# Optimization experiments

Measured on AMD Instinct MI355X. Metric: run time of the kernel, lower is better.

Reference implementation:

```python
import jax, jax.numpy as jnp
import numpy as np

DN = ('NCDHW', 'OIDHW', 'NCDHW')

def conv3(x, w):
    # 3x3x3 VALID stencil conv: [1,1,D+2,H+2,W+2] -> [1,1,D,H,W]
    return jax.lax.conv_general_dilated(x, w, (1, 1, 1), 'VALID', dimension_numbers=DN)

def conv_res(x, w):
    # 2x2x2 stride-2 restriction
    return jax.lax.conv_general_dilated(x, w, (2, 2, 2), 'VALID', dimension_numbers=DN)

def prol(x):
    for ax in (2, 3, 4):
        x = jnp.repeat(x, 2, axis=ax)
    return x

def with_halo(x, factor=1.0):
    # apply_BC_* + halo_exchange on one device: edge-replicate a 1-cell halo,
    # optionally scaled by `factor` (apply_BC_u uses -1.0 -> no-slip wall).
    p = jnp.pad(x, ((0, 0), (0, 0), (1, 1), (1, 1), (1, 1)), mode='edge')
    if factor != 1.0:
        interior = jnp.pad(jnp.ones_like(x), ((0, 0), (0, 0), (1, 1), (1, 1), (1, 1)))
        p = p * (interior + factor * (1.0 - interior))
    return p

def pad0(x):
    # apply_BC_cw: zero halo for the multigrid correction
    return jnp.pad(x, ((0, 0), (0, 0), (1, 1), (1, 1), (1, 1)))


def setup_inputs() -> dict:
    key = jax.random.key(0)
    ks = jax.random.split(key, 12)
    D = 128
    shp = (1, 1, D, D, D)
    f32 = jnp.float32
    values_u = jax.random.normal(ks[0], shp, f32)
    values_v = jax.random.normal(ks[1], shp, f32)
    values_w = jax.random.normal(ks[2], shp, f32)
    values_p = jax.random.normal(ks[3], shp, f32)
    sigma = jax.random.uniform(ks[4], shp, f32)
    kshape = (1, 1, 3, 3, 3)
    w_xadv = 0.1 * jax.random.normal(ks[5], kshape, f32)
    w_yadv = 0.1 * jax.random.normal(ks[6], kshape, f32)
    w_zadv = 0.1 * jax.random.normal(ks[7], kshape, f32)
    w_diff = 0.1 * jax.random.normal(ks[8], kshape, f32)
    wA = 0.1 * jax.random.normal(ks[9], kshape, f32)
    wA = wA.at[0, 0, 1, 1, 1].add(-6.0)  # Laplacian-like diagonal so Jacobi division is stable
    w_res = 0.1 * jax.random.normal(ks[10], (1, 1, 2, 2, 2), f32)
    dt = 0.05 * jnp.ones((1,), f32)
    return dict(values_u=values_u, values_v=values_v, values_w=values_w,
                values_p=values_p, sigma=sigma, w_xadv=w_xadv, w_yadv=w_yadv,
                w_zadv=w_zadv, w_diff=w_diff, wA=wA, w_res=w_res, dt=dt,
                iteration=2, nlevel=9)


def reference(values_u, values_v, values_w, values_p, sigma, w_xadv, w_yadv,
              w_zadv, w_diff, wA, w_res, dt, iteration, nlevel):
    diag = wA[0, 0, 1, 1, 1]
    xadv = lambda t: conv3(t, w_xadv)
    yadv = lambda t: conv3(t, w_yadv)
    zadv = lambda t: conv3(t, w_zadv)
    diff = lambda t: conv3(t, w_diff)
    A = lambda t: conv3(t, wA)

    def solid(a, b, c):
        d = 1.0 + dt * sigma
        return a / d, b / d, c / d

    def PG(uu, vv, ww, u, v, w):
        # k_u/k_v/k_w are ones; k_uu/k_vv/k_ww are their BC+halo versions (also ones)
        k_h = with_halo(jnp.ones_like(u))
        k_u = 0.5 * (diff(uu) + diff(uu * k_h) - u * diff(k_h))
        k_v = 0.5 * (diff(vv) + diff(vv * k_h) - v * diff(k_h))
        k_w = 0.5 * (diff(ww) + diff(ww * k_h) - w * diff(k_h))
        return k_u, k_v, k_w

    def f_cycle_mg(uu, vv, wwh, p, pp):
        b = -(xadv(uu) + yadv(vv) + zadv(wwh)) / dt
        w_mg = jnp.zeros((1, 1, 1, 1, 1), p.dtype)
        r = b
        for _ in range(iteration):
            w_mg = jnp.zeros((1, 1, 1, 1, 1), p.dtype)
            r = A(pp) - b
            r_s = [r]
            for _i in range(1, nlevel - 1):
                r = conv_res(r, w_res)
                r_s.append(r)
            for i in reversed(range(1, nlevel - 1)):
                ww_ = pad0(w_mg)
                w_mg = w_mg - A(ww_) / diag + r_s[i] / diag
                w_mg = prol(w_mg)
            p = p - w_mg
            p = p - A(pp) / diag + b / diag
            pp = with_halo(p)
        return p, w_mg, r, pp

    u, v, w = solid(values_u, values_v, values_w)
    uu = with_halo(u, -1.0)
    vv = with_halo(v)
    wwh = with_halo(w)
    pp = with_halo(values_p)

    k_u, k_v, k_w = PG(uu, vv, wwh, u, v, w)
    b_u = u + 0.5 * (0.001 * k_u * dt - u * xadv(uu) * dt - v * yadv(uu) * dt - w * zadv(uu) * dt) - xadv(pp) * dt
    b_v = v + 0.5 * (0.001 * k_v * dt - u * xadv(vv) * dt - v * yadv(vv) * dt - w * zadv(vv) * dt) - yadv(pp) * dt
    b_w = w + 0.5 * (0.001 * k_w * dt - u * xadv(wwh) * dt - v * yadv(wwh) * dt - w * zadv(wwh) * dt) - zadv(pp) * dt
    b_u, b_v, b_w = solid(b_u, b_v, b_w)
    b_uu = with_halo(b_u, -1.0)
    b_vv = with_halo(b_v)
    b_ww = with_halo(b_w)

    k_u, k_v, k_w = PG(b_uu, b_vv, b_ww, b_u, b_v, b_w)
    u = u + 0.001 * k_u * dt - b_u * xadv(b_uu) * dt - b_v * yadv(b_uu) * dt - b_w * zadv(b_uu) * dt - xadv(pp) * dt
    v = v + 0.001 * k_v * dt - b_u * xadv(b_vv) * dt - b_v * yadv(b_vv) * dt - b_w * zadv(b_vv) * dt - yadv(pp) * dt
    w = w + 0.001 * k_w * dt - b_u * xadv(b_ww) * dt - b_v * yadv(b_ww) * dt - b_w * zadv(b_ww) * dt - zadv(pp) * dt
    u, v, w = solid(u, v, w)

    uu = with_halo(u, -1.0)
    vv = with_halo(v)
    wwh = with_halo(w)
    p, w_mg, r, pp = f_cycle_mg(uu, vv, wwh, values_p, pp)

    u = u - xadv(pp) * dt
    v = v - yadv(pp) * dt
    w = w - zadv(pp) * dt
    u, v, w = solid(u, v, w)
    return (u, v, w, p, w_mg, r)
```

## Files before the change

kernel.cpp:

```cpp
#include <hip/hip_runtime.h>


#define NN 128
#define NF (NN*NN*NN)


__device__ __forceinline__ void prep9(int z, int y, int rb[9], bool rn[9]) {
  int zi[3] = {z > 0 ? z-1 : 0, z, z < NN-1 ? z+1 : NN-1};
  int yi[3] = {y > 0 ? y-1 : 0, y, y < NN-1 ? y+1 : NN-1};
  bool zo[3] = {z == 0, false, z == NN-1};
  bool yo[3] = {y == 0, false, y == NN-1};
#pragma unroll
  for (int a = 0; a < 3; ++a)
#pragma unroll
    for (int b = 0; b < 3; ++b) {
      rb[a*3+b] = (zi[a]*NN + yi[b])*NN;
      rn[a*3+b] = zo[a] | yo[b];
    }
}


template<bool NEG>
__device__ __forceinline__ void sten_vel(
    const float* __restrict__ f, const int rb[9], const bool rn[9],
    bool lo, bool hi, int x0,
    const float* __restrict__ w0p, const float* __restrict__ w1p,
    const float* __restrict__ w2p, const float* __restrict__ w3p,
    float acc[4][4], float4* center) {
  const float* const Ws[4] = {w0p, w1p, w2p, w3p};
#pragma unroll
  for (int r = 0; r < 9; ++r) {
    int base = rb[r] + x0;
    float4 c = *(const float4*)(f + base);
    float m1 = f[base - (lo ? 0 : 1)];
    float p4 = f[base + (hi ? 3 : 4)];
    if (NEG) {
      float sr = rn[r] ? -1.f : 1.f;
      m1 *= (rn[r] | lo) ? -1.f : 1.f;
      p4 *= (rn[r] | hi) ? -1.f : 1.f;
      c.x *= sr; c.y *= sr; c.z *= sr; c.w *= sr;
    }
    if (r == 4 && center) *center = c;
    float t[6] = {m1, c.x, c.y, c.z, c.w, p4};
#pragma unroll
    for (int s = 0; s < 4; ++s) {
      const float* W = Ws[s];
      float a0 = W[r*3+0], a1 = W[r*3+1], a2 = W[r*3+2];
#pragma unroll
      for (int k = 0; k < 4; ++k)
        acc[s][k] = fmaf(a0, t[k], fmaf(a1, t[k+1], fmaf(a2, t[k+2], acc[s][k])));
    }
  }
}

__device__ __forceinline__ void sten_p3(
    const float* __restrict__ f, const int rb[9], const bool rn[9],
    bool lo, bool hi, int x0,
    const float* __restrict__ w0p, const float* __restrict__ w1p,
    const float* __restrict__ w2p, float acc[3][4]) {
  const float* const Ws[3] = {w0p, w1p, w2p};
#pragma unroll
  for (int r = 0; r < 9; ++r) {
    int base = rb[r] + x0;
    float4 c = *(const float4*)(f + base);
    float m1 = f[base - (lo ? 0 : 1)];
    float p4 = f[base + (hi ? 3 : 4)];
    float t[6] = {m1, c.x, c.y, c.z, c.w, p4};
#pragma unroll
    for (int s = 0; s < 3; ++s) {
      const float* W = Ws[s];
      float a0 = W[r*3+0], a1 = W[r*3+1], a2 = W[r*3+2];
#pragma unroll
      for (int k = 0; k < 4; ++k)
        acc[s][k] = fmaf(a0, t[k], fmaf(a1, t[k+1], fmaf(a2, t[k+2], acc[s][k])));
    }
  }
}


__global__ void __launch_bounds__(256) k_solid3(
    float* __restrict__ du, float* __restrict__ dv, float* __restrict__ dw,
    const float* __restrict__ su, const float* __restrict__ sv, const float* __restrict__ sw,
    const float* __restrict__ sg, const float* __restrict__ dtp) {
  int i = blockIdx.x*256 + threadIdx.x;
  if (i >= NF/4) return;
  float dt = dtp[0];
  float4 s4 = ((const float4*)sg)[i];
  float4 a4 = ((const float4*)su)[i];
  float4 b4 = ((const float4*)sv)[i];
  float4 c4 = ((const float4*)sw)[i];
  float4 d4 = make_float4(1.f + dt*s4.x, 1.f + dt*s4.y, 1.f + dt*s4.z, 1.f + dt*s4.w);
  ((float4*)du)[i] = make_float4(a4.x/d4.x, a4.y/d4.y, a4.z/d4.z, a4.w/d4.w);
  ((float4*)dv)[i] = make_float4(b4.x/d4.x, b4.y/d4.y, b4.z/d4.z, b4.w/d4.w);
  ((float4*)dw)[i] = make_float4(c4.x/d4.x, c4.y/d4.y, c4.z/d4.z, c4.w/d4.w);
}

__global__ void __launch_bounds__(256) k_mom3(
    float* __restrict__ du, float* __restrict__ dv, float* __restrict__ dw,
    const float* __restrict__ su, const float* __restrict__ sv, const float* __restrict__ sw,
    const float* __restrict__ qu, const float* __restrict__ qv, const float* __restrict__ qw,
    const float* __restrict__ pf, const float* __restrict__ sg,
    const float* __restrict__ wx, const float* __restrict__ wy,
    const float* __restrict__ wz, const float* __restrict__ wd,
    const float* __restrict__ dtp, float scale) {
  int x0 = threadIdx.x * 4;
  int y  = blockIdx.x * 8 + threadIdx.y;
  int z  = blockIdx.y;
  bool lo = (x0 == 0), hi = (x0 == NN-4);
  int rb[9]; bool rn[9];
  prep9(z, y, rb, rn);
  float dt = dtp[0];

  float aU[4][4] = {}, aV[4][4] = {}, aW[4][4] = {}, aP[3][4] = {};
  float4 uc, vc, wc;
  sten_vel<true >(su, rb, rn, lo, hi, x0, wx, wy, wz, wd, aU, &uc);
  sten_vel<false>(sv, rb, rn, lo, hi, x0, wx, wy, wz, wd, aV, &vc);
  sten_vel<false>(sw, rb, rn, lo, hi, x0, wx, wy, wz, wd, aW, &wc);
  sten_p3(pf, rb, rn, lo, hi, x0, wx, wy, wz, aP);

  float sw27 = 0.f;
#pragma unroll
  for (int j = 0; j < 27; ++j) sw27 += wd[j];

  int i4 = ((z*NN + y)*NN + x0) >> 2;
  float4 qu4 = ((const float4*)qu)[i4];
  float4 qv4 = ((const float4*)qv)[i4];
  float4 qw4 = ((const float4*)qw)[i4];
  float4 sg4 = ((const float4*)sg)[i4];
  float ucv[4] = {uc.x, uc.y, uc.z, uc.w};
  float vcv[4] = {vc.x, vc.y, vc.z, vc.w};
  float wcv[4] = {wc.x, wc.y, wc.z, wc.w};
  float qua[4] = {qu4.x, qu4.y, qu4.z, qu4.w};
  float qva[4] = {qv4.x, qv4.y, qv4.z, qv4.w};
  float qwa[4] = {qw4.x, qw4.y, qw4.z, qw4.w};
  float sga[4] = {sg4.x, sg4.y, sg4.z, sg4.w};
  float ou[4], ov[4], ow[4];
#pragma unroll
  for (int k = 0; k < 4; ++k) {
    float ku = aU[3][k] - 0.5f*sw27*ucv[k];
    float kv = aV[3][k] - 0.5f*sw27*vcv[k];
    float kw = aW[3][k] - 0.5f*sw27*wcv[k];
    float ru = qua[k] + scale*dt*(0.001f*ku - ucv[k]*aU[0][k] - vcv[k]*aU[1][k] - wcv[k]*aU[2][k]) - aP[0][k]*dt;
    float rv = qva[k] + scale*dt*(0.001f*kv - ucv[k]*aV[0][k] - vcv[k]*aV[1][k] - wcv[k]*aV[2][k]) - aP[1][k]*dt;
    float rw = qwa[k] + scale*dt*(0.001f*kw - ucv[k]*aW[0][k] - vcv[k]*aW[1][k] - wcv[k]*aW[2][k]) - aP[2][k]*dt;
    float d = 1.0f + dt*sga[k];
    ou[k] = ru/d; ov[k] = rv/d; ow[k] = rw/d;
  }
  ((float4*)du)[i4] = make_float4(ou[0], ou[1], ou[2], ou[3]);
  ((float4*)dv)[i4] = make_float4(ov[0], ov[1], ov[2], ov[3]);
  ((float4*)dw)[i4] = make_float4(ow[0], ow[1], ow[2], ow[3]);
}


__device__ __forceinline__ void row4(const float* __restrict__ f, int base,
                                     bool lo, bool hi, float t[4]) {
  float2 c = *(const float2*)(f + base);
  t[0] = f[base - (lo ? 0 : 1)];
  t[1] = c.x; t[2] = c.y;
  t[3] = f[base + (hi ? 1 : 2)];
}

__device__ __forceinline__ void prep16(int Z, int Y, int rb[16], bool rn[16]) {
  int z0 = 2*Z, y0 = 2*Y;
  int zi[4] = {z0 > 0 ? z0-1 : 0, z0, z0+1, z0+2 < NN ? z0+2 : NN-1};
  int yi[4] = {y0 > 0 ? y0-1 : 0, y0, y0+1, y0+2 < NN ? y0+2 : NN-1};
  bool zo[4] = {Z == 0, false, false, Z == 63};
  bool yo[4] = {Y == 0, false, false, Y == 63};
#pragma unroll
  for (int a = 0; a < 4; ++a)
#pragma unroll
    for (int b = 0; b < 4; ++b) {
      rb[a*4+b] = (zi[a]*NN + yi[b])*NN;
      rn[a*4+b] = zo[a] | yo[b];
    }
}

template<bool NEG>
__device__ __forceinline__ void load16(const float* __restrict__ f,
    const int rb[16], const bool rn[16], bool lo, bool hi, int x0, float t[16][4]) {
#pragma unroll
  for (int r = 0; r < 16; ++r) {
    row4(f, rb[r] + x0, lo, hi, t[r]);
    if (NEG) {
      float sr = rn[r] ? -1.f : 1.f;
      t[r][0] *= (rn[r] | lo) ? -1.f : 1.f;
      t[r][3] *= (rn[r] | hi) ? -1.f : 1.f;
      t[r][1] *= sr; t[r][2] *= sr;
    }
  }
}

__device__ __forceinline__ void dots8(const float t[16][4],
                                      const float* __restrict__ W, float s8[8]) {
#pragma unroll
  for (int dz = 0; dz < 2; ++dz)
#pragma unroll
    for (int dy = 0; dy < 2; ++dy)
#pragma unroll
      for (int dx = 0; dx < 2; ++dx) {
        float s = 0.f;
#pragma unroll
        for (int a = 0; a < 3; ++a)
#pragma unroll
          for (int b = 0; b < 3; ++b)
#pragma unroll
            for (int c = 0; c < 3; ++c)
              s = fmaf(W[(a*3+b)*3+c], t[(dz+a)*4 + dy+b][dx+c], s);
        s8[(dz*2+dy)*2+dx] += s;
      }
}

__global__ void __launch_bounds__(256) k_bdiv_resres(
    float* __restrict__ bb, float* __restrict__ rfine, float* __restrict__ rc1,
    const float* __restrict__ su, const float* __restrict__ sv, const float* __restrict__ sw,
    const float* __restrict__ pf,
    const float* __restrict__ wx, const float* __restrict__ wy, const float* __restrict__ wz,
    const float* __restrict__ wA, const float* __restrict__ wr,
    const float* __restrict__ dtp) {
  int i = blockIdx.x*256 + threadIdx.x;
  if (i >= 64*64*64) return;
  int X = i & 63, Y = (i >> 6) & 63, Z = i >> 12;
  bool lo = (X == 0), hi = (X == 63);
  int x0 = 2*X;
  int rb[16]; bool rn[16];
  prep16(Z, Y, rb, rn);
  float rdt = 1.0f / dtp[0];

  float s8[8] = {};
  {
    float t[16][4];
    load16<true >(su, rb, rn, lo, hi, x0, t); dots8(t, wx, s8);
  }
  {
    float t[16][4];
    load16<false>(sv, rb, rn, lo, hi, x0, t); dots8(t, wy, s8);
  }
  {
    float t[16][4];
    load16<false>(sw, rb, rn, lo, hi, x0, t); dots8(t, wz, s8);
  }
  float a8[8] = {};
  {
    float t[16][4];
    load16<false>(pf, rb, rn, lo, hi, x0, t); dots8(t, wA, a8);
  }
  float rsum = 0.f;
#pragma unroll
  for (int f = 0; f < 8; ++f) {
    int dz = f >> 2, dy = (f >> 1) & 1, dx = f & 1;
    float bcell = -s8[f] * rdt;
    float rcell = a8[f] - bcell;
    int idx = ((2*Z+dz)*NN + (2*Y+dy))*NN + x0 + dx;
    bb[idx] = bcell;
    rfine[idx] = rcell;
    rsum = fmaf(wr[(dz*2+dy)*2+dx], rcell, rsum);
  }
  rc1[i] = rsum;
}

__global__ void __launch_bounds__(256) k_resres1(
    float* __restrict__ rfine, float* __restrict__ rc1,
    const float* __restrict__ pf, const float* __restrict__ bb,
    const float* __restrict__ wA, const float* __restrict__ wr) {
  int i = blockIdx.x*256 + threadIdx.x;
  if (i >= 64*64*64) return;
  int X = i & 63, Y = (i >> 6) & 63, Z = i >> 12;
  bool lo = (X == 0), hi = (X == 63);
  int x0 = 2*X;
  int rb[16]; bool rn[16];
  prep16(Z, Y, rb, rn);
  float a8[8] = {};
  {
    float t[16][4];
    load16<false>(pf, rb, rn, lo, hi, x0, t); dots8(t, wA, a8);
  }
  float rsum = 0.f;
#pragma unroll
  for (int f = 0; f < 8; ++f) {
    int dz = f >> 2, dy = (f >> 1) & 1, dx = f & 1;
    int idx = ((2*Z+dz)*NN + (2*Y+dy))*NN + x0 + dx;
    float rcell = a8[f] - bb[idx];
    rfine[idx] = rcell;
    rsum = fmaf(wr[(dz*2+dy)*2+dx], rcell, rsum);
  }
  rc1[i] = rsum;
}

__global__ void __launch_bounds__(256) k_restrict(
    float* __restrict__ dst, const float* __restrict__ src,
    const float* __restrict__ wr, int no) {
  int i = blockIdx.x*256 + threadIdx.x;
  int n3 = no*no*no;
  if (i >= n3) return;
  int x = i % no; int t = i / no; int y = t % no; int z = t / no;
  int ni = 2*no;
  float s = 0.f;
#pragma unroll
  for (int a = 0; a < 2; ++a)
#pragma unroll
    for (int b = 0; b < 2; ++b)
#pragma unroll
      for (int c = 0; c < 2; ++c)
        s = fmaf(wr[(a*2+b)*2+c], src[((2*z+a)*ni + (2*y+b))*ni + (2*x+c)], s);
  dst[i] = s;
}

__device__ __forceinline__ float azb_prol(const float* __restrict__ wh, int hs, int s,
    int z, int y, int x, const float* __restrict__ wA) {
  float acc = 0.f;
#pragma unroll
  for (int a = 0; a < 3; ++a) { int zz = z + a - 1; if ((unsigned)zz >= (unsigned)s) continue;
#pragma unroll
    for (int b = 0; b < 3; ++b) { int yy = y + b - 1; if ((unsigned)yy >= (unsigned)s) continue;
#pragma unroll
      for (int c = 0; c < 3; ++c) { int xx = x + c - 1; if ((unsigned)xx >= (unsigned)s) continue;
        acc = fmaf(wA[(a*3+b)*3+c], wh[((zz>>1)*hs + (yy>>1))*hs + (xx>>1)], acc);
      } } }
  return acc;
}

__global__ void __launch_bounds__(512) k_mg_small(
    float* __restrict__ w16, float* __restrict__ r_o,
    const float* __restrict__ rc2,
    const float* __restrict__ wA, const float* __restrict__ wr) {
  __shared__ float r16[4096];
  __shared__ float r8[512];
  __shared__ float r4[64];
  __shared__ float r2[8];
  __shared__ float wa[512];
  __shared__ float wb[64];
  __shared__ float scal[2];
  int tid = threadIdx.x;
  float diag = wA[13];
  float wrl[8];
#pragma unroll
  for (int j = 0; j < 8; ++j) wrl[j] = wr[j];

  for (int j = tid; j < 4096; j += 512) {
    int x = j & 15, y = (j >> 4) & 15, z = j >> 8;
    float s = 0.f;
#pragma unroll
    for (int a = 0; a < 2; ++a)
#pragma unroll
      for (int b = 0; b < 2; ++b)
#pragma unroll
        for (int c = 0; c < 2; ++c)
          s = fmaf(wrl[(a*2+b)*2+c], rc2[((2*z+a)*32 + (2*y+b))*32 + (2*x+c)], s);
    r16[j] = s;
  }
  __syncthreads();
  {
    int j = tid;
    int x = j & 7, y = (j >> 3) & 7, z = j >> 6;
    float s = 0.f;
#pragma unroll
    for (int a = 0; a < 2; ++a)
#pragma unroll
      for (int b = 0; b < 2; ++b)
#pragma unroll
        for (int c = 0; c < 2; ++c)
          s = fmaf(wrl[(a*2+b)*2+c], r16[((2*z+a)*16 + (2*y+b))*16 + (2*x+c)], s);
    r8[j] = s;
  }
  __syncthreads();
  if (tid < 64) {
    int x = tid & 3, y = (tid >> 2) & 3, z = tid >> 4;
    float s = 0.f;
#pragma unroll
    for (int a = 0; a < 2; ++a)
#pragma unroll
      for (int b = 0; b < 2; ++b)
#pragma unroll
        for (int c = 0; c < 2; ++c)
          s = fmaf(wrl[(a*2+b)*2+c], r8[((2*z+a)*8 + (2*y+b))*8 + (2*x+c)], s);
    r4[tid] = s;
  }
  __syncthreads();
  if (tid < 8) {
    int x = tid & 1, y = (tid >> 1) & 1, z = tid >> 2;
    float s = 0.f;
#pragma unroll
    for (int a = 0; a < 2; ++a)
#pragma unroll
      for (int b = 0; b < 2; ++b)
#pragma unroll
        for (int c = 0; c < 2; ++c)
          s = fmaf(wrl[(a*2+b)*2+c], r4[((2*z+a)*4 + (2*y+b))*4 + (2*x+c)], s);
    r2[tid] = s;
  }
  __syncthreads();
  if (tid == 0) {
    float s = 0.f;
#pragma unroll
    for (int j = 0; j < 8; ++j) s = fmaf(wrl[j], r2[j], s);
    scal[0] = s;
    r_o[0] = s;
    scal[1] = s / diag;
  }
  __syncthreads();
  if (tid < 8) {
    int x = tid & 1, y = (tid >> 1) & 1, z = tid >> 2;
    float wp = scal[1];
    float az = azb_prol(&scal[1], 1, 2, z, y, x, wA);
    wa[tid] = wp - az/diag + r2[tid]/diag;
  }
  __syncthreads();
  if (tid < 64) {
    int x = tid & 3, y = (tid >> 2) & 3, z = tid >> 4;
    float wp = wa[((z>>1)*2 + (y>>1))*2 + (x>>1)];
    float az = azb_prol(wa, 2, 4, z, y, x, wA);
    wb[tid] = wp - az/diag + r4[tid]/diag;
  }
  __syncthreads();
  {
    int j = tid;
    int x = j & 7, y = (j >> 3) & 7, z = j >> 6;
    float wp = wb[((z>>1)*4 + (y>>1))*4 + (x>>1)];
    float az = azb_prol(wb, 4, 8, z, y, x, wA);
    wa[j] = wp - az/diag + r8[j]/diag;
  }
  __syncthreads();
  for (int j = tid; j < 4096; j += 512) {
    int x = j & 15, y = (j >> 4) & 15, z = j >> 8;
    float wp = wa[((z>>1)*8 + (y>>1))*8 + (x>>1)];
    float az = azb_prol(wa, 8, 16, z, y, x, wA);
    w16[j] = wp - az/diag + r16[j]/diag;
  }
}

__global__ void __launch_bounds__(256) k_coarse_step(
    float* __restrict__ wout, const float* __restrict__ wh,
    const float* __restrict__ rl, const float* __restrict__ wA, int s) {
  int i = blockIdx.x*256 + threadIdx.x;
  int n3 = s*s*s;
  if (i >= n3) return;
  int x = i % s; int t = i / s; int y = t % s; int z = t / s;
  int hs = s >> 1;
  float diag = wA[13];
  float wp = wh[((z>>1)*hs + (y>>1))*hs + (x>>1)];
  float az = azb_prol(wh, hs, s, z, y, x, wA);
  wout[i] = wp - az/diag + rl[i]/diag;
}

__global__ void __launch_bounds__(256) k_pupd4(
    float* __restrict__ pdst, float* __restrict__ wmgo,
    const float* __restrict__ psrc, const float* __restrict__ rfine,
    const float* __restrict__ w64, const float* __restrict__ wA, int writeWmg) {
  int i4 = blockIdx.x*256 + threadIdx.x;
  if (i4 >= NF/4) return;
  int i = i4*4;
  int x = i & (NN-1); int t = i >> 7; int y = t & (NN-1); int z = t >> 7;
  float rdiag = 1.0f / wA[13];
  float2 w2 = *(const float2*)(w64 + ((size_t)(z>>1)*64 + (y>>1))*64 + (x>>1));
  float4 ps = ((const float4*)psrc)[i4];
  float4 rf = ((const float4*)rfine)[i4];
  float4 o = make_float4(ps.x - w2.x - rf.x*rdiag,
                         ps.y - w2.x - rf.y*rdiag,
                         ps.z - w2.y - rf.z*rdiag,
                         ps.w - w2.y - rf.w*rdiag);
  ((float4*)pdst)[i4] = o;
  if (writeWmg) ((float4*)wmgo)[i4] = make_float4(w2.x, w2.x, w2.y, w2.y);
}

__global__ void __launch_bounds__(256) k_proj3(
    float* __restrict__ u, float* __restrict__ v, float* __restrict__ w,
    const float* __restrict__ pf, const float* __restrict__ sg,
    const float* __restrict__ wx, const float* __restrict__ wy,
    const float* __restrict__ wz, const float* __restrict__ dtp) {
  int x0 = threadIdx.x * 4;
  int y  = blockIdx.x * 8 + threadIdx.y;
  int z  = blockIdx.y;
  bool lo = (x0 == 0), hi = (x0 == NN-4);
  int rb[9]; bool rn[9];
  prep9(z, y, rb, rn);
  float aP[3][4] = {};
  sten_p3(pf, rb, rn, lo, hi, x0, wx, wy, wz, aP);
  float dt = dtp[0];
  int i4 = ((z*NN + y)*NN + x0) >> 2;
  float4 u4 = ((const float4*)u)[i4];
  float4 v4 = ((const float4*)v)[i4];
  float4 w4 = ((const float4*)w)[i4];
  float4 sg4 = ((const float4*)sg)[i4];
  float ua[4] = {u4.x, u4.y, u4.z, u4.w};
  float va[4] = {v4.x, v4.y, v4.z, v4.w};
  float wa[4] = {w4.x, w4.y, w4.z, w4.w};
  float sa[4] = {sg4.x, sg4.y, sg4.z, sg4.w};
  float ou[4], ov[4], ow[4];
#pragma unroll
  for (int k = 0; k < 4; ++k) {
    float d = 1.0f + dt*sa[k];
    ou[k] = (ua[k] - aP[0][k]*dt)/d;
    ov[k] = (va[k] - aP[1][k]*dt)/d;
    ow[k] = (wa[k] - aP[2][k]*dt)/d;
  }
  ((float4*)u)[i4] = make_float4(ou[0], ou[1], ou[2], ou[3]);
  ((float4*)v)[i4] = make_float4(ov[0], ov[1], ov[2], ov[3]);
  ((float4*)w)[i4] = make_float4(ow[0], ow[1], ow[2], ow[3]);
}


extern "C" void kernel_launch(void* const* d_in, const int* in_sizes, int n_in,
                              void* d_out, int out_size, void* d_ws, size_t ws_size,
                              hipStream_t stream) {
  const float* values_u = (const float*)d_in[0];
  const float* values_v = (const float*)d_in[1];
  const float* values_w = (const float*)d_in[2];
  const float* values_p = (const float*)d_in[3];
  const float* sigma    = (const float*)d_in[4];
  const float* wx       = (const float*)d_in[5];
  const float* wy       = (const float*)d_in[6];
  const float* wz       = (const float*)d_in[7];
  const float* wd       = (const float*)d_in[8];
  const float* wA       = (const float*)d_in[9];
  const float* wr       = (const float*)d_in[10];
  const float* dtp      = (const float*)d_in[11];

  float* out   = (float*)d_out;
  float* u_o   = out;
  float* v_o   = out + (size_t)NF;
  float* w_o   = out + (size_t)2*NF;
  float* p_o   = out + (size_t)3*NF;
  float* wmg_o = out + (size_t)4*NF;
  float* r_o   = out + (size_t)5*NF;

  float* ws    = (float*)d_ws;
  float* f0    = ws;
  float* f1    = f0 + (size_t)NF;
  float* f2    = f1 + (size_t)NF;
  float* bws   = f2 + (size_t)NF;
  float* rfine = bws + (size_t)NF;
  float* pbuf  = rfine + (size_t)NF;
  float* rc1   = pbuf + (size_t)NF;
  float* rc2   = rc1 + 262144;
  float* w16   = rc2 + 32768;
  float* w32   = w16 + 4096;
  float* w64   = w32 + 32768;

  const int TB = 256;
  dim3 blkS(32, 8, 1);
  dim3 grdS(16, 128, 1);

  k_solid3<<<NF/4/TB, TB, 0, stream>>>(u_o, v_o, w_o, values_u, values_v, values_w, sigma, dtp);
  k_mom3<<<grdS, blkS, 0, stream>>>(f0, f1, f2, u_o, v_o, w_o, u_o, v_o, w_o,
                                    values_p, sigma, wx, wy, wz, wd, dtp, 0.5f);
  k_mom3<<<grdS, blkS, 0, stream>>>(u_o, v_o, w_o, f0, f1, f2, u_o, v_o, w_o,
                                    values_p, sigma, wx, wy, wz, wd, dtp, 1.0f);

  k_bdiv_resres<<<1024, TB, 0, stream>>>(bws, rfine, rc1, u_o, v_o, w_o, values_p,
                                         wx, wy, wz, wA, wr, dtp);
  k_restrict<<<128, TB, 0, stream>>>(rc2, rc1, wr, 32);
  k_mg_small<<<1, 512, 0, stream>>>(w16, r_o, rc2, wA, wr);
  k_coarse_step<<<128, TB, 0, stream>>>(w32, w16, rc2, wA, 32);
  k_coarse_step<<<1024, TB, 0, stream>>>(w64, w32, rc1, wA, 64);
  k_pupd4<<<NF/4/TB, TB, 0, stream>>>(pbuf, wmg_o, values_p, rfine, w64, wA, 0);

  k_resres1<<<1024, TB, 0, stream>>>(rfine, rc1, pbuf, bws, wA, wr);
  k_restrict<<<128, TB, 0, stream>>>(rc2, rc1, wr, 32);
  k_mg_small<<<1, 512, 0, stream>>>(w16, r_o, rc2, wA, wr);
  k_coarse_step<<<128, TB, 0, stream>>>(w32, w16, rc2, wA, 32);
  k_coarse_step<<<1024, TB, 0, stream>>>(w64, w32, rc1, wA, 64);
  k_pupd4<<<NF/4/TB, TB, 0, stream>>>(p_o, wmg_o, pbuf, rfine, w64, wA, 1);

  k_proj3<<<grdS, blkS, 0, stream>>>(u_o, v_o, w_o, p_o, sigma, wx, wy, wz, dtp);
}
```

Baseline: 242.9 us.

## Split momentum kernels per velocity component and stream z-planes in restriction stencil

Each fused three-component momentum kernel is replaced by three per-component launches (six in total). Each launch computes one 4-weight velocity stencil plus a single pressure-gradient stencil, which cuts live accumulators and register pressure so more waves can be resident. The cost is re-reading the pressure field, sigma and the neighbouring velocity centres in every launch, plus extra launch overhead. Separately, the residual/restriction stencil now loads and consumes one z-plane of rows at a time instead of holding a 16x4 tile per field, further lowering register usage.

```diff
diff --git a/kernel.cpp b/kernel.cpp
--- a/kernel.cpp
+++ b/kernel.cpp
@@ -19,9 +19,8 @@
     }
 }
 
-
 template<bool NEG>
-__device__ __forceinline__ void sten_vel(
+__device__ __forceinline__ void sten4(
     const float* __restrict__ f, const int rb[9], const bool rn[9],
     bool lo, bool hi, int x0,
     const float* __restrict__ w0p, const float* __restrict__ w1p,
@@ -53,8 +52,25 @@
   }
 }
 
+__device__ __forceinline__ void sten1(
+    const float* __restrict__ f, const int rb[9],
+    bool lo, bool hi, int x0, const float* __restrict__ W, float acc[4]) {
+#pragma unroll
+  for (int r = 0; r < 9; ++r) {
+    int base = rb[r] + x0;
+    float4 c = *(const float4*)(f + base);
+    float m1 = f[base - (lo ? 0 : 1)];
+    float p4 = f[base + (hi ? 3 : 4)];
+    float t[6] = {m1, c.x, c.y, c.z, c.w, p4};
+    float a0 = W[r*3+0], a1 = W[r*3+1], a2 = W[r*3+2];
+#pragma unroll
+    for (int k = 0; k < 4; ++k)
+      acc[k] = fmaf(a0, t[k], fmaf(a1, t[k+1], fmaf(a2, t[k+2], acc[k])));
+  }
+}
+
 __device__ __forceinline__ void sten_p3(
-    const float* __restrict__ f, const int rb[9], const bool rn[9],
+    const float* __restrict__ f, const int rb[9],
     bool lo, bool hi, int x0,
     const float* __restrict__ w0p, const float* __restrict__ w1p,
     const float* __restrict__ w2p, float acc[3][4]) {
@@ -95,13 +111,15 @@
   ((float4*)dw)[i] = make_float4(c4.x/d4.x, c4.y/d4.y, c4.z/d4.z, c4.w/d4.w);
 }
 
-__global__ void __launch_bounds__(256) k_mom3(
-    float* __restrict__ du, float* __restrict__ dv, float* __restrict__ dw,
-    const float* __restrict__ su, const float* __restrict__ sv, const float* __restrict__ sw,
-    const float* __restrict__ qu, const float* __restrict__ qv, const float* __restrict__ qw,
-    const float* __restrict__ pf, const float* __restrict__ sg,
+template<int CI, bool QALIAS>
+__global__ void __launch_bounds__(256) k_momc(
+    float* __restrict__ dst,
+    const float* __restrict__ sq, const float* __restrict__ pf,
+    const float* __restrict__ a1p, const float* __restrict__ a2p,
+    const float* __restrict__ qb, const float* __restrict__ sg,
     const float* __restrict__ wx, const float* __restrict__ wy,
     const float* __restrict__ wz, const float* __restrict__ wd,
+    const float* __restrict__ wp,
     const float* __restrict__ dtp, float scale) {
   int x0 = threadIdx.x * 4;
   int y  = blockIdx.x * 8 + threadIdx.y;
@@ -110,45 +128,43 @@
   int rb[9]; bool rn[9];
   prep9(z, y, rb, rn);
   float dt = dtp[0];
-
-  float aU[4][4] = {}, aV[4][4] = {}, aW[4][4] = {}, aP[3][4] = {};
-  float4 uc, vc, wc;
-  sten_vel<true >(su, rb, rn, lo, hi, x0, wx, wy, wz, wd, aU, &uc);
-  sten_vel<false>(sv, rb, rn, lo, hi, x0, wx, wy, wz, wd, aV, &vc);
-  sten_vel<false>(sw, rb, rn, lo, hi, x0, wx, wy, wz, wd, aW, &wc);
-  sten_p3(pf, rb, rn, lo, hi, x0, wx, wy, wz, aP);
+  int i4 = ((z*NN + y)*NN + x0) >> 2;
+
+  float4 a1_4 = ((const float4*)a1p)[i4];
+  float4 a2_4 = ((const float4*)a2p)[i4];
+  float4 sg4  = ((const float4*)sg)[i4];
+  float4 qb4;
+  if (!QALIAS) qb4 = ((const float4*)qb)[i4];
+
+  float acc[4][4] = {};
+  float accP[4]   = {};
+  float4 cen;
+  sten4<(CI==0)>(sq, rb, rn, lo, hi, x0, wx, wy, wz, wd, acc, &cen);
+  sten1(pf, rb, lo, hi, x0, wp, accP);
 
   float sw27 = 0.f;
 #pragma unroll
   for (int j = 0; j < 27; ++j) sw27 += wd[j];
 
-  int i4 = ((z*NN + y)*NN + x0) >> 2;
-  float4 qu4 = ((const float4*)qu)[i4];
-  float4 qv4 = ((const float4*)qv)[i4];
-  float4 qw4 = ((const float4*)qw)[i4];
-  float4 sg4 = ((const float4*)sg)[i4];
-  float ucv[4] = {uc.x, uc.y, uc.z, uc.w};
-  float vcv[4] = {vc.x, vc.y, vc.z, vc.w};
-  float wcv[4] = {wc.x, wc.y, wc.z, wc.w};
-  float qua[4] = {qu4.x, qu4.y, qu4.z, qu4.w};
-  float qva[4] = {qv4.x, qv4.y, qv4.z, qv4.w};
-  float qwa[4] = {qw4.x, qw4.y, qw4.z, qw4.w};
-  float sga[4] = {sg4.x, sg4.y, sg4.z, sg4.w};
-  float ou[4], ov[4], ow[4];
+  float cenv[4] = {cen.x, cen.y, cen.z, cen.w};
+  float a1v[4] = {a1_4.x, a1_4.y, a1_4.z, a1_4.w};
+  float a2v[4] = {a2_4.x, a2_4.y, a2_4.z, a2_4.w};
+  float sgv[4] = {sg4.x, sg4.y, sg4.z, sg4.w};
+  float o[4];
 #pragma unroll
   for (int k = 0; k < 4; ++k) {
-    float ku = aU[3][k] - 0.5f*sw27*ucv[k];
-    float kv = aV[3][k] - 0.5f*sw27*vcv[k];
-    float kw = aW[3][k] - 0.5f*sw27*wcv[k];
-    float ru = qua[k] + scale*dt*(0.001f*ku - ucv[k]*aU[0][k] - vcv[k]*aU[1][k] - wcv[k]*aU[2][k]) - aP[0][k]*dt;
-    float rv = qva[k] + scale*dt*(0.001f*kv - ucv[k]*aV[0][k] - vcv[k]*aV[1][k] - wcv[k]*aV[2][k]) - aP[1][k]*dt;
-    float rw = qwa[k] + scale*dt*(0.001f*kw - ucv[k]*aW[0][k] - vcv[k]*aW[1][k] - wcv[k]*aW[2][k]) - aP[2][k]*dt;
-    float d = 1.0f + dt*sga[k];
-    ou[k] = ru/d; ov[k] = rv/d; ow[k] = rw/d;
-  }
-  ((float4*)du)[i4] = make_float4(ou[0], ou[1], ou[2], ou[3]);
-  ((float4*)dv)[i4] = make_float4(ov[0], ov[1], ov[2], ov[3]);
-  ((float4*)dw)[i4] = make_float4(ow[0], ow[1], ow[2], ow[3]);
+    float cu, cv, cw;
+    if (CI == 0) { cu = cenv[k]; cv = a1v[k]; cw = a2v[k]; }
+    else if (CI == 1) { cu = a1v[k]; cv = cenv[k]; cw = a2v[k]; }
+    else { cu = a1v[k]; cv = a2v[k]; cw = cenv[k]; }
+    float kk = acc[3][k] - 0.5f*sw27*cenv[k];
+    float q = QALIAS ? cenv[k]
+            : (k==0 ? qb4.x : k==1 ? qb4.y : k==2 ? qb4.z : qb4.w);
+    float r = q + scale*dt*(0.001f*kk - cu*acc[0][k] - cv*acc[1][k] - cw*acc[2][k])
+            - accP[k]*dt;
+    o[k] = r / (1.0f + dt*sgv[k]);
+  }
+  ((float4*)dst)[i4] = make_float4(o[0], o[1], o[2], o[3]);
 }
 
 
@@ -176,38 +192,41 @@
 }
 
 template<bool NEG>
-__device__ __forceinline__ void load16(const float* __restrict__ f,
-    const int rb[16], const bool rn[16], bool lo, bool hi, int x0, float t[16][4]) {
-#pragma unroll
-  for (int r = 0; r < 16; ++r) {
-    row4(f, rb[r] + x0, lo, hi, t[r]);
-    if (NEG) {
-      float sr = rn[r] ? -1.f : 1.f;
-      t[r][0] *= (rn[r] | lo) ? -1.f : 1.f;
-      t[r][3] *= (rn[r] | hi) ? -1.f : 1.f;
-      t[r][1] *= sr; t[r][2] *= sr;
-    }
-  }
-}
-
-__device__ __forceinline__ void dots8(const float t[16][4],
-                                      const float* __restrict__ W, float s8[8]) {
-#pragma unroll
-  for (int dz = 0; dz < 2; ++dz)
-#pragma unroll
-    for (int dy = 0; dy < 2; ++dy)
-#pragma unroll
-      for (int dx = 0; dx < 2; ++dx) {
-        float s = 0.f;
-#pragma unroll
-        for (int a = 0; a < 3; ++a)
-#pragma unroll
-          for (int b = 0; b < 3; ++b)
-#pragma unroll
-            for (int c = 0; c < 3; ++c)
-              s = fmaf(W[(a*3+b)*3+c], t[(dz+a)*4 + dy+b][dx+c], s);
-        s8[(dz*2+dy)*2+dx] += s;
+__device__ __forceinline__ void cc_acc(
+    const float* __restrict__ f, const float* __restrict__ W,
+    const int rb[16], const bool rn[16], bool lo, bool hi, int x0,
+    float out8[8]) {
+#pragma unroll
+  for (int zp = 0; zp < 4; ++zp) {
+    float t[4][4];
+#pragma unroll
+    for (int yp = 0; yp < 4; ++yp) {
+      row4(f, rb[zp*4+yp] + x0, lo, hi, t[yp]);
+      if (NEG) {
+        bool rno = rn[zp*4+yp];
+        float sr = rno ? -1.f : 1.f;
+        t[yp][1] *= sr; t[yp][2] *= sr;
+        t[yp][0] *= (rno | lo) ? -1.f : 1.f;
+        t[yp][3] *= (rno | hi) ? -1.f : 1.f;
       }
+    }
+#pragma unroll
+    for (int dz = 0; dz < 2; ++dz) {
+      int a = zp - dz;
+      if (a < 0 || a > 2) continue;
+#pragma unroll
+      for (int oy = 0; oy < 2; ++oy)
+#pragma unroll
+        for (int b = 0; b < 3; ++b) {
+          const float* tr = t[oy + b];
+          float w0 = W[(a*3+b)*3+0], w1 = W[(a*3+b)*3+1], w2 = W[(a*3+b)*3+2];
+#pragma unroll
+          for (int dx = 0; dx < 2; ++dx)
+            out8[(dz*2+oy)*2+dx] =
+              fmaf(w0, tr[dx], fmaf(w1, tr[dx+1], fmaf(w2, tr[dx+2], out8[(dz*2+oy)*2+dx])));
+        }
+    }
+  }
 }
 
 __global__ void __launch_bounds__(256) k_bdiv_resres(
@@ -227,23 +246,12 @@
   float rdt = 1.0f / dtp[0];
 
   float s8[8] = {};
-  {
-    float t[16][4];
-    load16<true >(su, rb, rn, lo, hi, x0, t); dots8(t, wx, s8);
-  }
-  {
-    float t[16][4];
-    load16<false>(sv, rb, rn, lo, hi, x0, t); dots8(t, wy, s8);
-  }
-  {
-    float t[16][4];
-    load16<false>(sw, rb, rn, lo, hi, x0, t); dots8(t, wz, s8);
-  }
+  cc_acc<true >(su, wx, rb, rn, lo, hi, x0, s8);
+  cc_acc<false>(sv, wy, rb, rn, lo, hi, x0, s8);
+  cc_acc<false>(sw, wz, rb, rn, lo, hi, x0, s8);
   float a8[8] = {};
-  {
-    float t[16][4];
-    load16<false>(pf, rb, rn, lo, hi, x0, t); dots8(t, wA, a8);
-  }
+  cc_acc<false>(pf, wA, rb, rn, lo, hi, x0, a8);
+
   float rsum = 0.f;
 #pragma unroll
   for (int f = 0; f < 8; ++f) {
@@ -270,10 +278,7 @@
   int rb[16]; bool rn[16];
   prep16(Z, Y, rb, rn);
   float a8[8] = {};
-  {
-    float t[16][4];
-    load16<false>(pf, rb, rn, lo, hi, x0, t); dots8(t, wA, a8);
-  }
+  cc_acc<false>(pf, wA, rb, rn, lo, hi, x0, a8);
   float rsum = 0.f;
 #pragma unroll
   for (int f = 0; f < 8; ++f) {
@@ -474,7 +479,7 @@
   int rb[9]; bool rn[9];
   prep9(z, y, rb, rn);
   float aP[3][4] = {};
-  sten_p3(pf, rb, rn, lo, hi, x0, wx, wy, wz, aP);
+  sten_p3(pf, rb, lo, hi, x0, wx, wy, wz, aP);
   float dt = dtp[0];
   int i4 = ((z*NN + y)*NN + x0) >> 2;
   float4 u4 = ((const float4*)u)[i4];
@@ -541,10 +546,19 @@
   dim3 grdS(16, 128, 1);
 
   k_solid3<<<NF/4/TB, TB, 0, stream>>>(u_o, v_o, w_o, values_u, values_v, values_w, sigma, dtp);
-  k_mom3<<<grdS, blkS, 0, stream>>>(f0, f1, f2, u_o, v_o, w_o, u_o, v_o, w_o,
-                                    values_p, sigma, wx, wy, wz, wd, dtp, 0.5f);
-  k_mom3<<<grdS, blkS, 0, stream>>>(u_o, v_o, w_o, f0, f1, f2, u_o, v_o, w_o,
-                                    values_p, sigma, wx, wy, wz, wd, dtp, 1.0f);
+
+  k_momc<0, true><<<grdS, blkS, 0, stream>>>(f0, u_o, values_p, v_o, w_o, u_o, sigma,
+                                             wx, wy, wz, wd, wx, dtp, 0.5f);
+  k_momc<1, true><<<grdS, blkS, 0, stream>>>(f1, v_o, values_p, u_o, w_o, v_o, sigma,
+                                             wx, wy, wz, wd, wy, dtp, 0.5f);
+  k_momc<2, true><<<grdS, blkS, 0, stream>>>(f2, w_o, values_p, u_o, v_o, w_o, sigma,
+                                             wx, wy, wz, wd, wz, dtp, 0.5f);
+  k_momc<0, false><<<grdS, blkS, 0, stream>>>(u_o, f0, values_p, f1, f2, u_o, sigma,
+                                              wx, wy, wz, wd, wx, dtp, 1.0f);
+  k_momc<1, false><<<grdS, blkS, 0, stream>>>(v_o, f1, values_p, f0, f2, v_o, sigma,
+                                              wx, wy, wz, wd, wy, dtp, 1.0f);
+  k_momc<2, false><<<grdS, blkS, 0, stream>>>(w_o, f2, values_p, f0, f1, w_o, sigma,
+                                              wx, wy, wz, wd, wz, dtp, 1.0f);
 
   k_bdiv_resres<<<1024, TB, 0, stream>>>(bws, rfine, rc1, u_o, v_o, w_o, values_p,
                                          wx, wy, wz, wA, wr, dtp);
```

Measured after the change: 297.5 us. 1.22x slower.
